# Kernel optimization log

Measured on AMD Instinct MI355X. Metric: run time of the kernel, lower is better.

## Reference

```python
import jax, jax.numpy as jnp
import numpy as np

B, N, NODE_DIM = 64, 64, 192
H = 256          # node_hidden_dim
PDIM = 64        # property_embedding_dim
NUM_EDGE_TYPE = 5
T = 4            # message-passing rounds
E = 16384        # total edges (flattened batched graph)
E_SEL = 65536    # selected candidate pairs


def setup_inputs() -> dict:
    key = jax.random.key(0)
    ks = jax.random.split(key, 24)
    def g(k, shape, scale=0.05):
        return jax.random.normal(k, shape, dtype=jnp.float32) * scale
    inp = {
        "x": jax.random.normal(ks[0], (B, N, NODE_DIM), dtype=jnp.float32),
        "edge_index": jax.random.randint(ks[1], (2, E), 0, B * N, dtype=jnp.int32),
        "edge_attr": jax.random.uniform(ks[2], (E, NUM_EDGE_TYPE), dtype=jnp.float32),
        "props": jax.random.normal(ks[3], (B, 1), dtype=jnp.float32),
        "sel_b": jax.random.randint(ks[4], (E_SEL,), 0, B, dtype=jnp.int32),
        "sel_i": jax.random.randint(ks[5], (E_SEL,), 0, N, dtype=jnp.int32),
        "sel_j": jax.random.randint(ks[6], (E_SEL,), 0, N, dtype=jnp.int32),
        "golden_edge": jax.random.randint(ks[7], (E_SEL,), 0, NUM_EDGE_TYPE, dtype=jnp.int32),
        # parameters
        "W_prop": g(ks[8], (1, PDIM)), "b_prop": jnp.zeros((PDIM,), jnp.float32),
        "W_in": g(ks[9], (NODE_DIM, H)), "b_in": jnp.zeros((H,), jnp.float32),
        "W_msg": g(ks[10], (H + NUM_EDGE_TYPE, H)), "b_msg": jnp.zeros((H,), jnp.float32),
        "W_upd": g(ks[11], (2 * H, H)), "b_upd": jnp.zeros((H,), jnp.float32),
        "W_add": g(ks[12], (H + PDIM, H)), "b_add": jnp.zeros((H,), jnp.float32),
        "W1": g(ks[13], (2 * H, H)), "b1": jnp.zeros((H,), jnp.float32),
        "W2": g(ks[14], (H, H)), "b2": jnp.zeros((H,), jnp.float32),
        "W3": g(ks[15], (H, 2 * H)), "b3": jnp.zeros((2 * H,), jnp.float32),
        "W_out": g(ks[16], (2 * H, NUM_EDGE_TYPE)), "b_out": jnp.zeros((NUM_EDGE_TYPE,), jnp.float32),
    }
    return inp


def reference(x, edge_index, edge_attr, props, sel_b, sel_i, sel_j, golden_edge,
              W_prop, b_prop, W_in, b_in, W_msg, b_msg, W_upd, b_upd,
              W_add, b_add, W1, b1, W2, b2, W3, b3, W_out, b_out):
    BN = B * N
    node_x = x.reshape(BN, NODE_DIM)
    src, dst = edge_index[0], edge_index[1]

    # --- GNN node embedding (t rounds of message passing, opaque Encoder.embed_node) ---
    h = jax.nn.relu(node_x @ W_in + b_in)                       # [BN, H]
    for _ in range(T):
        msg_in = jnp.concatenate([h[src], edge_attr], axis=-1)  # [E, H+num_edge_type]
        msg = jax.nn.relu(msg_in @ W_msg + b_msg)               # [E, H]
        agg = jax.ops.segment_sum(msg, dst, num_segments=BN)    # [BN, H]
        h = jax.nn.relu(jnp.concatenate([h, agg], axis=-1) @ W_upd + b_upd)

    node_emb = h.reshape(B, N, H)

    # --- property conditioning + addition linear ---
    prop = props @ W_prop + b_prop                               # [B, PDIM]
    propp = jnp.broadcast_to(prop[:, None, :], (B, N, PDIM))
    node_embg = jnp.concatenate([node_emb, propp], axis=-1) @ W_add + b_add  # [B, N, H]

    # --- gather selected (src, dst) pairs directly (equiv. to repeat_interleave + boolean mask) ---
    flat = node_embg.reshape(BN, H)
    src_e = flat[sel_b * N + sel_i]                              # [E_SEL, H]
    dst_e = flat[sel_b * N + sel_j]                              # [E_SEL, H]
    pair = jnp.concatenate([src_e, dst_e], axis=-1)              # [E_SEL, 2H]

    # --- edge predictor MLP (3 layers, ReLU between) + output linear ---
    h1 = jax.nn.relu(pair @ W1 + b1)
    h2 = jax.nn.relu(h1 @ W2 + b2)
    h3 = h2 @ W3 + b3
    logits = h3 @ W_out + b_out                                  # [E_SEL, num_edge_type]

    # --- cross entropy (mean) ---
    logp = jax.nn.log_softmax(logits, axis=-1)
    loss = -jnp.mean(jnp.take_along_axis(logp, golden_edge[:, None].astype(jnp.int32), axis=-1))
    return loss
```

## Files before the change

### kernel.cpp

```cpp
#include <hip/hip_runtime.h>
#include <math.h>

#define BN 4096
#define N_PER_B 64
#define NE 16384
#define NSEL 65536
#define NET 5
#define PD 64
#define H1STR 260
#define FSTR 264
#define PTILES 2

typedef float f32x4 __attribute__((ext_vector_type(4)));
typedef float f32x16 __attribute__((ext_vector_type(16)));
typedef short short8 __attribute__((ext_vector_type(8)));
typedef short short4v __attribute__((ext_vector_type(4)));

__device__ __forceinline__ unsigned short f2bf(float f) {
    unsigned int u = __builtin_bit_cast(unsigned int, f);
    u += 0x7fff + ((u >> 16) & 1);
    return (unsigned short)(u >> 16);
}
__device__ __forceinline__ float bf_lo(unsigned int u) {
    return __builtin_bit_cast(float, u << 16);
}
__device__ __forceinline__ float bf_hi(unsigned int u) {
    return __builtin_bit_cast(float, u & 0xffff0000u);
}
__device__ __forceinline__ unsigned int pack2(float a, float b) {
    return (unsigned)f2bf(a) | ((unsigned)f2bf(b) << 16);
}
__device__ __forceinline__ short8 ld_frag(const unsigned short* p) {
    const short4v lo = *(const short4v*)(p);
    const short4v hi = *(const short4v*)(p + 4);
    return __builtin_shufflevector(lo, hi, 0, 1, 2, 3, 4, 5, 6, 7);
}
__device__ __forceinline__ unsigned int addrelu2(unsigned int a, unsigned int b, unsigned int c) {
    const float lo = fmaxf(bf_lo(a) + bf_lo(b) + bf_lo(c), 0.f);
    const float hi = fmaxf(bf_hi(a) + bf_hi(b) + bf_hi(c), 0.f);
    return pack2(lo, hi);
}

__global__ __launch_bounds__(256) void k_hist(const int* __restrict__ eidx,
                                              int* __restrict__ deg)
{
    const int e = blockIdx.x * 256 + threadIdx.x;
    atomicAdd(&deg[eidx[NE + e]], 1);
}

__global__ __launch_bounds__(256) void csr_scan(const int* __restrict__ deg,
                                                int* __restrict__ row_start,
                                                int* __restrict__ cursor)
{
    __shared__ int sums[256];
    const int tid = threadIdx.x;
    const int base = tid * 16;
    int local[16];
    int s = 0;
    #pragma unroll
    for (int i = 0; i < 16; ++i) { local[i] = s; s += deg[base + i]; }
    sums[tid] = s;
    __syncthreads();
    for (int off = 1; off < 256; off <<= 1) {
        const int v = sums[tid];
        const int add = (tid >= off) ? sums[tid - off] : 0;
        __syncthreads();
        sums[tid] = v + add;
        __syncthreads();
    }
    const int offset = (tid == 0) ? 0 : sums[tid - 1];
    #pragma unroll
    for (int i = 0; i < 16; ++i) {
        const int v = offset + local[i];
        row_start[base + i] = v;
        cursor[base + i] = v;
    }
    if (tid == 255) row_start[4096] = NE;
}

__global__ __launch_bounds__(256) void csr_scatter(const int* __restrict__ eidx,
                                                   int* __restrict__ cursor,
                                                   int* __restrict__ srcs,
                                                   int* __restrict__ epos)
{
    const int e = blockIdx.x * 256 + threadIdx.x;
    const int pos = atomicAdd(&cursor[eidx[NE + e]], 1);
    srcs[pos] = eidx[e];
    epos[e] = pos;
}

__global__ __launch_bounds__(256) void k_pre(
    const float* __restrict__ W_in, const float* __restrict__ W_msg,
    const float* __restrict__ W_upd, const float* __restrict__ W_add,
    const float* __restrict__ W1, const float* __restrict__ W2,
    const float* __restrict__ W3, const float* __restrict__ b3,
    const float* __restrict__ W_out, const float* __restrict__ b_out,
    const float* __restrict__ props, const float* __restrict__ W_prop,
    const float* __restrict__ b_prop, const float* __restrict__ b_add,
    const float* __restrict__ b_msg, const float* __restrict__ eattr,
    const int* __restrict__ epos,
    unsigned short* __restrict__ wbf, unsigned short* __restrict__ WfT,
    float* __restrict__ bfv, float* __restrict__ prop_add,
    unsigned short* __restrict__ ETc)
{
    __shared__ __align__(16) char smem[16704];
    const int blk = blockIdx.x;
    const int tid = threadIdx.x;

    if (blk < 128) {
        float (*s)[65] = (float(*)[65])smem;
        const int wsel = blk >> 4;
        const int sub = blk & 15;
        const float* src; unsigned short* dst; int K = 256;
        switch (wsel) {
            case 0: src = W_in;              dst = wbf;                         K = 192; break;
            case 1: src = W_msg;             dst = wbf + 49152;                 break;
            case 2: src = W_upd;             dst = wbf + 49152 + 65536;         break;
            case 3: src = W_upd + 256 * 256; dst = wbf + 49152 + 2 * 65536;     break;
            case 4: src = W_add;             dst = wbf + 49152 + 3 * 65536;     break;
            case 5: src = W1;                dst = wbf + 49152 + 4 * 65536;     break;
            case 6: src = W1 + 256 * 256;    dst = wbf + 49152 + 5 * 65536;     break;
            default: src = W2;               dst = wbf + 49152 + 6 * 65536;     break;
        }
        const int k0 = (sub >> 2) * 64;
        const int n0 = (sub & 3) * 64;
        if (k0 >= K) return;
        const int tn = tid & 63;
        const int tg = tid >> 6;
        #pragma unroll
        for (int i = 0; i < 16; ++i) {
            const int kk = tg * 16 + i;
            s[kk][tn] = src[(size_t)(k0 + kk) * 256 + n0 + tn];
        }
        __syncthreads();
        #pragma unroll
        for (int i = 0; i < 16; ++i) {
            const int nn = tg * 16 + i;
            dst[(size_t)(n0 + nn) * K + k0 + tn] = f2bf(s[tn][nn]);
        }
    } else if (blk < 192) {
        const int b = blk - 128;
        const float pv = props[b];
        float acc = b_add[tid];
        for (int p = 0; p < PD; ++p) {
            const float e = fmaf(pv, W_prop[p], b_prop[p]);
            acc = fmaf(e, W_add[(256 + p) * 256 + tid], acc);
        }
        prop_add[b * 256 + tid] = acc;
    } else if (blk < 449) {
        float* part = (float*)smem;
        const int cb = blk - 192;
        float acc[NET] = {0.f, 0.f, 0.f, 0.f, 0.f};
        #pragma unroll
        for (int rep = 0; rep < 2; ++rep) {
            const int j = rep * 256 + tid;
            const float wv = (cb < 256) ? W3[(size_t)cb * 512 + j] : b3[j];
            #pragma unroll
            for (int t = 0; t < NET; ++t) acc[t] = fmaf(wv, W_out[j * NET + t], acc[t]);
        }
        #pragma unroll
        for (int t = 0; t < NET; ++t)
            for (int off = 32; off >= 1; off >>= 1) acc[t] += __shfl_down(acc[t], off);
        if ((tid & 63) == 0) {
            #pragma unroll
            for (int t = 0; t < NET; ++t) part[(tid >> 6) * NET + t] = acc[t];
        }
        __syncthreads();
        if (tid == 0) {
            float s[NET];
            #pragma unroll
            for (int t = 0; t < NET; ++t)
                s[t] = part[t] + part[NET + t] + part[2 * NET + t] + part[3 * NET + t];
            if (cb < 256) {
                #pragma unroll
                for (int t = 0; t < NET; ++t) WfT[t * 256 + cb] = f2bf(s[t]);
                #pragma unroll
                for (int t = NET; t < 16; ++t) WfT[t * 256 + cb] = 0;
            } else {
                #pragma unroll
                for (int t = 0; t < NET; ++t) bfv[t] = s[t] + b_out[t];
            }
        }
    } else {
        float* ea = (float*)smem;
        int* eposs = (int*)(smem + 2560 + 64);
        const int eb = (blk - 449) * 128;
        if (tid < 160)
            *(float4*)&ea[tid * 4] = *(const float4*)(eattr + (size_t)eb * 5 + tid * 4);
        if (tid < 128) eposs[tid] = epos[eb + tid];
        __syncthreads();
        const float* Wme = W_msg + 256 * 256;
        const float w0 = Wme[0 * 256 + tid];
        const float w1 = Wme[1 * 256 + tid];
        const float w2 = Wme[2 * 256 + tid];
        const float w3 = Wme[3 * 256 + tid];
        const float w4 = Wme[4 * 256 + tid];
        const float bm = b_msg[tid];
        for (int i = 0; i < 128; ++i) {
            const float* a = ea + i * 5;
            float v = bm;
            v = fmaf(a[0], w0, v); v = fmaf(a[1], w1, v); v = fmaf(a[2], w2, v);
            v = fmaf(a[3], w3, v); v = fmaf(a[4], w4, v);
            ETc[(size_t)eposs[i] * 256 + tid] = f2bf(v);
        }
    }
}

__global__ __launch_bounds__(1024) void fstep(
    const float* __restrict__ x, const unsigned short* __restrict__ hbuf,
    const unsigned short* __restrict__ Pin, const unsigned short* __restrict__ ETc,
    const int* __restrict__ row_start, const int* __restrict__ srcs,
    const unsigned short* __restrict__ WaT, const unsigned short* __restrict__ WbT,
    const float* __restrict__ bias1,
    const unsigned short* __restrict__ Wp2T, const float* __restrict__ prop_add,
    const unsigned short* __restrict__ W1aT, const unsigned short* __restrict__ W1bT,
    unsigned short* __restrict__ hout, unsigned short* __restrict__ out1,
    unsigned short* __restrict__ out2, int mode)
{
    __shared__ __align__(16) unsigned short Hg[16 * FSTR];
    __shared__ __align__(16) unsigned short Ag[16 * FSTR];
    __shared__ __align__(16) unsigned short Hs[16 * FSTR];
    __shared__ __align__(16) unsigned short H2s[16 * FSTR];
    const int tid = threadIdx.x;
    const int w = tid >> 6;
    const int lane = tid & 63;
    const int q = lane >> 4;
    const int tx = lane & 15;
    const int m0 = blockIdx.x * 16;
    const int col = w * 16 + tx;

    if (mode != 0) {
        {
            const int r = tid >> 6;
            const int c4 = (tid & 63) * 4;
            *(uint2*)&Hg[r * FSTR + c4] =
                *(const uint2*)(hbuf + (size_t)(m0 + r) * 256 + c4);
        }
        {
            const int node = m0 + w;
            const int beg = row_start[node];
            const int end = row_start[node + 1];
            const int c = lane * 4;
            float a0 = 0.f, a1 = 0.f, a2 = 0.f, a3 = 0.f;
            for (int idx = beg; idx < end; ++idx) {
                const int src = srcs[idx];
                const uint2 pu = *(const uint2*)(Pin + (size_t)src * 256 + c);
                const uint2 eu = *(const uint2*)(ETc + (size_t)idx * 256 + c);
                a0 += fmaxf(bf_lo(pu.x) + bf_lo(eu.x), 0.f);
                a1 += fmaxf(bf_hi(pu.x) + bf_hi(eu.x), 0.f);
                a2 += fmaxf(bf_lo(pu.y) + bf_lo(eu.y), 0.f);
                a3 += fmaxf(bf_hi(pu.y) + bf_hi(eu.y), 0.f);
            }
            uint2 o; o.x = pack2(a0, a1); o.y = pack2(a2, a3);
            *(uint2*)&Ag[w * FSTR + c] = o;
        }
        __syncthreads();
    }

    f32x4 acc = (f32x4)0.f;
    if (mode == 0) {
        #pragma unroll
        for (int s = 0; s < 6; ++s) {
            const int k0 = s * 32;
            const float* ap = x + (size_t)(m0 + tx) * 192 + k0 + q * 8;
            const float4 v0 = *(const float4*)ap;
            const float4 v1 = *(const float4*)(ap + 4);
            short8 af;
            af[0] = (short)f2bf(v0.x); af[1] = (short)f2bf(v0.y);
            af[2] = (short)f2bf(v0.z); af[3] = (short)f2bf(v0.w);
            af[4] = (short)f2bf(v1.x); af[5] = (short)f2bf(v1.y);
            af[6] = (short)f2bf(v1.z); af[7] = (short)f2bf(v1.w);
            const short8 bfr = *(const short8*)(WaT + (size_t)col * 192 + k0 + q * 8);
            acc = __builtin_amdgcn_mfma_f32_16x16x32_bf16(af, bfr, acc, 0, 0, 0);
        }
    } else {
        #pragma unroll
        for (int s = 0; s < 8; ++s) {
            const int k0 = s * 32;
            const short8 af = *(const short8*)&Hg[tx * FSTR + k0 + q * 8];
            const short8 bfr = *(const short8*)(WaT + (size_t)col * 256 + k0 + q * 8);
            acc = __builtin_amdgcn_mfma_f32_16x16x32_bf16(af, bfr, acc, 0, 0, 0);
        }
        #pragma unroll
        for (int s = 0; s < 8; ++s) {
            const int k0 = s * 32;
            const short8 af = *(const short8*)&Ag[tx * FSTR + k0 + q * 8];
            const short8 bfr = *(const short8*)(WbT + (size_t)col * 256 + k0 + q * 8);
            acc = __builtin_amdgcn_mfma_f32_16x16x32_bf16(af, bfr, acc, 0, 0, 0);
        }
    }
    {
        const float bv = bias1[col];
        #pragma unroll
        for (int r = 0; r < 4; ++r) {
            const int row = q * 4 + r;
            const unsigned short us = f2bf(fmaxf(acc[r] + bv, 0.f));
            Hs[row * FSTR + col] = us;
            if (mode < 2) hout[(size_t)(m0 + row) * 256 + col] = us;
        }
    }
    __syncthreads();

    acc = (f32x4)0.f;
    #pragma unroll
    for (int s = 0; s < 8; ++s) {
        const int k0 = s * 32;
        const short8 af = *(const short8*)&Hs[tx * FSTR + k0 + q * 8];
        const short8 bfr = *(const short8*)(Wp2T + (size_t)col * 256 + k0 + q * 8);
        acc = __builtin_amdgcn_mfma_f32_16x16x32_bf16(af, bfr, acc, 0, 0, 0);
    }
    if (mode < 2) {
        #pragma unroll
        for (int r = 0; r < 4; ++r)
            out1[(size_t)(m0 + q * 4 + r) * 256 + col] = f2bf(acc[r]);
        return;
    }
    {
        const float pv = prop_add[(m0 >> 6) * 256 + col];
        #pragma unroll
        for (int r = 0; r < 4; ++r)
            H2s[(q * 4 + r) * FSTR + col] = f2bf(acc[r] + pv);
    }
    __syncthreads();

    for (int which = 0; which < 2; ++which) {
        const unsigned short* WT = which ? W1bT : W1aT;
        unsigned short* op = which ? out2 : out1;
        acc = (f32x4)0.f;
        #pragma unroll
        for (int s = 0; s < 8; ++s) {
            const int k0 = s * 32;
            const short8 af = *(const short8*)&H2s[tx * FSTR + k0 + q * 8];
            const short8 bfr = *(const short8*)(WT + (size_t)col * 256 + k0 + q * 8);
            acc = __builtin_amdgcn_mfma_f32_16x16x32_bf16(af, bfr, acc, 0, 0, 0);
        }
        #pragma unroll
        for (int r = 0; r < 4; ++r)
            op[(size_t)(m0 + q * 4 + r) * 256 + col] = f2bf(acc[r]);
    }
}

__global__ __launch_bounds__(512, 2) void pair_k(
    const unsigned short* __restrict__ A1t, const unsigned short* __restrict__ A2t,
    const float* __restrict__ b1, const unsigned short* __restrict__ W2T,
    const float* __restrict__ b2, const unsigned short* __restrict__ WfT,
    const float* __restrict__ bfv,
    const int* __restrict__ sel_b, const int* __restrict__ sel_i,
    const int* __restrict__ sel_j, const int* __restrict__ golden,
    float* __restrict__ out)
{
    __shared__ __align__(16) unsigned short sbuf[64 * H1STR];
    __shared__ __align__(16) unsigned short b1s[256];
    __shared__ float Lg[64 * 8];
    __shared__ int sidx[64 * PTILES], didx[64 * PTILES], gold[64 * PTILES];

    const int tid = threadIdx.x;
    const int w = tid >> 6;
    const int lane = tid & 63;
    const int q = lane >> 4;
    const int tx = lane & 15;
    const int m = lane & 31;
    const int hh = lane >> 5;
    const int e0 = blockIdx.x * 64 * PTILES;

    if (tid < 64 * PTILES) {
        const int e = e0 + tid;
        const int b = sel_b[e];
        sidx[tid] = b * N_PER_B + sel_i[e];
        didx[tid] = b * N_PER_B + sel_j[e];
        gold[tid] = golden[e];
    }
    if (tid < 256) b1s[tid] = f2bf(b1[tid]);

    short8 Breg[16];
    {
        const unsigned short* bb = W2T + (size_t)(w * 32 + m) * 256 + hh * 8;
        #pragma unroll
        for (int s = 0; s < 16; ++s)
            Breg[s] = *(const short8*)(bb + s * 16);
    }
    __syncthreads();

    float total = 0.f;

    for (int t = 0; t < PTILES; ++t) {
        {
            const int hw = tid >> 5;
            #pragma unroll
            for (int j = 0; j < 4; ++j) {
                const int p = j * 16 + hw;
                const unsigned short* r1 = A1t + (size_t)sidx[t * 64 + p] * 256 + m * 8;
                const unsigned short* r2 = A2t + (size_t)didx[t * 64 + p] * 256 + m * 8;
                const uint4 u1 = *(const uint4*)r1;
                const uint4 u2 = *(const uint4*)r2;
                const uint4 ub = *(const uint4*)(b1s + m * 8);
                uint2 lo2, hi2;
                lo2.x = addrelu2(u1.x, u2.x, ub.x);
                lo2.y = addrelu2(u1.y, u2.y, ub.y);
                hi2.x = addrelu2(u1.z, u2.z, ub.z);
                hi2.y = addrelu2(u1.w, u2.w, ub.w);
                unsigned short* dbase = sbuf + p * H1STR + m * 8;
                *(uint2*)(dbase) = lo2;
                *(uint2*)(dbase + 4) = hi2;
            }
        }
        __syncthreads();

        f32x16 acc0 = (f32x16)0.f;
        f32x16 acc1 = (f32x16)0.f;
        {
            const unsigned short* a0row = sbuf + (size_t)m * H1STR + hh * 8;
            const unsigned short* a1row = a0row + 32 * H1STR;
            #pragma unroll
            for (int s = 0; s < 16; ++s) {
                const short8 af0 = ld_frag(a0row + s * 16);
                acc0 = __builtin_amdgcn_mfma_f32_32x32x16_bf16(af0, Breg[s], acc0, 0, 0, 0);
                const short8 af1 = ld_frag(a1row + s * 16);
                acc1 = __builtin_amdgcn_mfma_f32_32x32x16_bf16(af1, Breg[s], acc1, 0, 0, 0);
            }
        }
        __syncthreads();

        {
            const int col = w * 32 + m;
            const float bv = b2[col];
            #pragma unroll
            for (int reg = 0; reg < 16; ++reg) {
                const int prow = (reg & 3) + 8 * (reg >> 2) + 4 * hh;
                sbuf[prow * H1STR + col] = f2bf(fmaxf(acc0[reg] + bv, 0.f));
                sbuf[(32 + prow) * H1STR + col] = f2bf(fmaxf(acc1[reg] + bv, 0.f));
            }
        }
        __syncthreads();

        if (w < 4) {
            f32x4 accL = (f32x4)0.f;
            const unsigned short* a2row = sbuf + (size_t)(w * 16 + tx) * H1STR + q * 8;
            const unsigned short* bWf = WfT + (size_t)tx * 256 + q * 8;
            #pragma unroll
            for (int s = 0; s < 8; ++s) {
                const short8 af = ld_frag(a2row + s * 32);
                const short8 bfr = *(const short8*)(bWf + s * 32);
                accL = __builtin_amdgcn_mfma_f32_16x16x32_bf16(af, bfr, accL, 0, 0, 0);
            }
            if (tx < NET) {
                const float bb = bfv[tx];
                #pragma unroll
                for (int reg = 0; reg < 4; ++reg)
                    Lg[(w * 16 + q * 4 + reg) * 8 + tx] = accL[reg] + bb;
            }
        }
        __syncthreads();

        if (tid < 64) {
            float lg[NET];
            #pragma unroll
            for (int tt = 0; tt < NET; ++tt) lg[tt] = Lg[tid * 8 + tt];
            float mx = lg[0];
            #pragma unroll
            for (int tt = 1; tt < NET; ++tt) mx = fmaxf(mx, lg[tt]);
            float s = 0.f;
            #pragma unroll
            for (int tt = 0; tt < NET; ++tt) s += expf(lg[tt] - mx);
            float ls = mx + logf(s) - lg[gold[t * 64 + tid]];
            #pragma unroll
            for (int off = 32; off >= 1; off >>= 1) ls += __shfl_xor(ls, off);
            total += ls;
        }
        __syncthreads();
    }

    if (tid == 0) atomicAdd(out, total * (1.0f / NSEL));
}

extern "C" void kernel_launch(void* const* d_in, const int* in_sizes, int n_in,
                              void* d_out, int out_size, void* d_ws, size_t ws_size,
                              hipStream_t stream) {
    (void)in_sizes; (void)n_in; (void)out_size; (void)ws_size;
    const float* x      = (const float*)d_in[0];
    const int*   eidx   = (const int*)d_in[1];
    const float* eattr  = (const float*)d_in[2];
    const float* props  = (const float*)d_in[3];
    const int*   sel_b  = (const int*)d_in[4];
    const int*   sel_i  = (const int*)d_in[5];
    const int*   sel_j  = (const int*)d_in[6];
    const int*   golden = (const int*)d_in[7];
    const float* W_prop = (const float*)d_in[8];
    const float* b_prop = (const float*)d_in[9];
    const float* W_in   = (const float*)d_in[10];
    const float* b_in   = (const float*)d_in[11];
    const float* W_msg  = (const float*)d_in[12];
    const float* b_msg  = (const float*)d_in[13];
    const float* W_upd  = (const float*)d_in[14];
    const float* b_upd  = (const float*)d_in[15];
    const float* W_add  = (const float*)d_in[16];
    const float* b_add  = (const float*)d_in[17];
    const float* W1     = (const float*)d_in[18];
    const float* b1     = (const float*)d_in[19];
    const float* W2     = (const float*)d_in[20];
    const float* b2     = (const float*)d_in[21];
    const float* W3     = (const float*)d_in[22];
    const float* b3     = (const float*)d_in[23];
    const float* W_out  = (const float*)d_in[24];
    const float* b_out  = (const float*)d_in[25];

    const size_t SEG = (size_t)BN * 256;
    unsigned short* P0   = (unsigned short*)d_ws;
    unsigned short* P1   = P0 + SEG;
    unsigned short* hA   = P1 + SEG;
    unsigned short* hB   = hA + SEG;
    unsigned short* ETc  = hB + SEG;
    unsigned short* wbf  = ETc + (size_t)NE * 256;
    unsigned short* W_inT  = wbf;
    unsigned short* WmT    = wbf + 49152;
    unsigned short* WuaT   = WmT + 65536;
    unsigned short* WubT   = WuaT + 65536;
    unsigned short* W_addT = WubT + 65536;
    unsigned short* W1aT   = W_addT + 65536;
    unsigned short* W1bT   = W1aT + 65536;
    unsigned short* W2T    = W1bT + 65536;
    unsigned short* WfT    = W2T + 65536;
    float* prop_add = (float*)(WfT + 4096);
    float* bfv = prop_add + 64 * 256;
    int* deg       = (int*)(bfv + 16);
    int* row_start = deg + 4096;
    int* cursor    = row_start + 4104;
    int* srcs      = cursor + 4096;
    int* epos      = srcs + NE;

    hipMemsetAsync(deg, 0, 4096 * sizeof(int), stream);
    k_hist<<<NE / 256, 256, 0, stream>>>(eidx, deg);
    csr_scan<<<1, 256, 0, stream>>>(deg, row_start, cursor);
    csr_scatter<<<NE / 256, 256, 0, stream>>>(eidx, cursor, srcs, epos);
    k_pre<<<577, 256, 0, stream>>>(W_in, W_msg, W_upd, W_add, W1, W2, W3, b3,
                                   W_out, b_out, props, W_prop, b_prop, b_add,
                                   b_msg, eattr, epos, wbf, WfT, bfv, prop_add, ETc);

    fstep<<<256, 1024, 0, stream>>>(x, nullptr, nullptr, ETc, row_start, srcs,
                                    W_inT, nullptr, b_in, WmT, nullptr, nullptr, nullptr,
                                    hA, P0, nullptr, 0);
    fstep<<<256, 1024, 0, stream>>>(nullptr, hA, P0, ETc, row_start, srcs,
                                    WuaT, WubT, b_upd, WmT, nullptr, nullptr, nullptr,
                                    hB, P1, nullptr, 1);
    fstep<<<256, 1024, 0, stream>>>(nullptr, hB, P1, ETc, row_start, srcs,
                                    WuaT, WubT, b_upd, WmT, nullptr, nullptr, nullptr,
                                    hA, P0, nullptr, 1);
    fstep<<<256, 1024, 0, stream>>>(nullptr, hA, P0, ETc, row_start, srcs,
                                    WuaT, WubT, b_upd, WmT, nullptr, nullptr, nullptr,
                                    hB, P1, nullptr, 1);
    fstep<<<256, 1024, 0, stream>>>(nullptr, hB, P1, ETc, row_start, srcs,
                                    WuaT, WubT, b_upd, W_addT, prop_add, W1aT, W1bT,
                                    nullptr, P0, hA, 2);

    hipMemsetAsync(d_out, 0, sizeof(float), stream);
    pair_k<<<NSEL / (64 * PTILES), 512, 0, stream>>>(P0, hA, b1, W2T, b2, WfT, bfv,
                                    sel_b, sel_i, sel_j, golden, (float*)d_out);
}
```

Baseline: 254.2 us.

## Fuse CSR build into one kernel, fold output memset, unroll edge gather

Replaces the memset, histogram, single-block scan and scatter kernels with one 64-block kernel. Each block scans all destinations, counts edges that fall below its 64-node range to get its starting offset, and scatters its own edges using shared-memory atomics. The output zeroing moves into k_pre so one memset launch disappears, and the message-aggregation gather loop is unrolled by four so more loads are in flight. The trade-off is that every CSR block reads the whole edge list twice, the scatter order inside a node stays nondeterministic, and float summation order changes.

```diff
diff --git a/kernel.cpp b/kernel.cpp
--- a/kernel.cpp
+++ b/kernel.cpp
@@ -41,52 +41,55 @@
     return pack2(lo, hi);
 }
 
-__global__ __launch_bounds__(256) void k_hist(const int* __restrict__ eidx,
-                                              int* __restrict__ deg)
+__global__ __launch_bounds__(256) void csr_fused(const int* __restrict__ eidx,
+                                                 int* __restrict__ row_start,
+                                                 int* __restrict__ srcs,
+                                                 int* __restrict__ epos)
 {
-    const int e = blockIdx.x * 256 + threadIdx.x;
-    atomicAdd(&deg[eidx[NE + e]], 1);
-}
-
-__global__ __launch_bounds__(256) void csr_scan(const int* __restrict__ deg,
-                                                int* __restrict__ row_start,
-                                                int* __restrict__ cursor)
-{
-    __shared__ int sums[256];
+    __shared__ int own[64];
+    __shared__ int red[256];
     const int tid = threadIdx.x;
-    const int base = tid * 16;
-    int local[16];
-    int s = 0;
-    #pragma unroll
-    for (int i = 0; i < 16; ++i) { local[i] = s; s += deg[base + i]; }
-    sums[tid] = s;
+    const int blk = blockIdx.x;
+    const int lo = blk * 64;
+
+    if (tid < 64) own[tid] = 0;
     __syncthreads();
-    for (int off = 1; off < 256; off <<= 1) {
-        const int v = sums[tid];
-        const int add = (tid >= off) ? sums[tid - off] : 0;
-        __syncthreads();
-        sums[tid] = v + add;
-        __syncthreads();
-    }
-    const int offset = (tid == 0) ? 0 : sums[tid - 1];
-    #pragma unroll
-    for (int i = 0; i < 16; ++i) {
-        const int v = offset + local[i];
-        row_start[base + i] = v;
-        cursor[base + i] = v;
-    }
-    if (tid == 255) row_start[4096] = NE;
-}
-
-__global__ __launch_bounds__(256) void csr_scatter(const int* __restrict__ eidx,
-                                                   int* __restrict__ cursor,
-                                                   int* __restrict__ srcs,
-                                                   int* __restrict__ epos)
-{
-    const int e = blockIdx.x * 256 + threadIdx.x;
-    const int pos = atomicAdd(&cursor[eidx[NE + e]], 1);
-    srcs[pos] = eidx[e];
-    epos[e] = pos;
+
+    int cnt = 0;
+    #pragma unroll 4
+    for (int i = 0; i < 64; ++i) {
+        const int d = eidx[NE + i * 256 + tid];
+        if (d < lo) ++cnt;
+        else if (d < lo + 64) atomicAdd(&own[d - lo], 1);
+    }
+    red[tid] = cnt;
+    __syncthreads();
+    for (int off = 128; off >= 1; off >>= 1) {
+        if (tid < off) red[tid] += red[tid + off];
+        __syncthreads();
+    }
+    if (tid == 0) {
+        int acc = red[0];
+        for (int i = 0; i < 64; ++i) {
+            const int d = own[i];
+            own[i] = acc;
+            row_start[lo + i] = acc;
+            acc += d;
+        }
+        if (blk == 63) row_start[4096] = NE;
+    }
+    __syncthreads();
+
+    #pragma unroll 4
+    for (int i = 0; i < 64; ++i) {
+        const int e = i * 256 + tid;
+        const int d = eidx[NE + e];
+        if (d >= lo && d < lo + 64) {
+            const int pos = atomicAdd(&own[d - lo], 1);
+            srcs[pos] = eidx[e];
+            epos[e] = pos;
+        }
+    }
 }
 
 __global__ __launch_bounds__(256) void k_pre(
@@ -101,11 +104,13 @@
     const int* __restrict__ epos,
     unsigned short* __restrict__ wbf, unsigned short* __restrict__ WfT,
     float* __restrict__ bfv, float* __restrict__ prop_add,
-    unsigned short* __restrict__ ETc)
+    unsigned short* __restrict__ ETc, float* __restrict__ out)
 {
     __shared__ __align__(16) char smem[16704];
     const int blk = blockIdx.x;
     const int tid = threadIdx.x;
+
+    if (blk == 0 && tid == 0) out[0] = 0.f;
 
     if (blk < 128) {
         float (*s)[65] = (float(*)[65])smem;
@@ -242,7 +247,28 @@
             const int end = row_start[node + 1];
             const int c = lane * 4;
             float a0 = 0.f, a1 = 0.f, a2 = 0.f, a3 = 0.f;
-            for (int idx = beg; idx < end; ++idx) {
+            int idx = beg;
+            for (; idx + 3 < end; idx += 4) {
+                const int s0 = srcs[idx], s1 = srcs[idx + 1];
+                const int s2 = srcs[idx + 2], s3 = srcs[idx + 3];
+                const uint2 p0 = *(const uint2*)(Pin + (size_t)s0 * 256 + c);
+                const uint2 p1 = *(const uint2*)(Pin + (size_t)s1 * 256 + c);
+                const uint2 p2 = *(const uint2*)(Pin + (size_t)s2 * 256 + c);
+                const uint2 p3 = *(const uint2*)(Pin + (size_t)s3 * 256 + c);
+                const uint2 e0 = *(const uint2*)(ETc + (size_t)idx * 256 + c);
+                const uint2 e1 = *(const uint2*)(ETc + (size_t)(idx + 1) * 256 + c);
+                const uint2 e2 = *(const uint2*)(ETc + (size_t)(idx + 2) * 256 + c);
+                const uint2 e3 = *(const uint2*)(ETc + (size_t)(idx + 3) * 256 + c);
+                a0 += fmaxf(bf_lo(p0.x) + bf_lo(e0.x), 0.f) + fmaxf(bf_lo(p1.x) + bf_lo(e1.x), 0.f)
+                    + fmaxf(bf_lo(p2.x) + bf_lo(e2.x), 0.f) + fmaxf(bf_lo(p3.x) + bf_lo(e3.x), 0.f);
+                a1 += fmaxf(bf_hi(p0.x) + bf_hi(e0.x), 0.f) + fmaxf(bf_hi(p1.x) + bf_hi(e1.x), 0.f)
+                    + fmaxf(bf_hi(p2.x) + bf_hi(e2.x), 0.f) + fmaxf(bf_hi(p3.x) + bf_hi(e3.x), 0.f);
+                a2 += fmaxf(bf_lo(p0.y) + bf_lo(e0.y), 0.f) + fmaxf(bf_lo(p1.y) + bf_lo(e1.y), 0.f)
+                    + fmaxf(bf_lo(p2.y) + bf_lo(e2.y), 0.f) + fmaxf(bf_lo(p3.y) + bf_lo(e3.y), 0.f);
+                a3 += fmaxf(bf_hi(p0.y) + bf_hi(e0.y), 0.f) + fmaxf(bf_hi(p1.y) + bf_hi(e1.y), 0.f)
+                    + fmaxf(bf_hi(p2.y) + bf_hi(e2.y), 0.f) + fmaxf(bf_hi(p3.y) + bf_hi(e3.y), 0.f);
+            }
+            for (; idx < end; ++idx) {
                 const int src = srcs[idx];
                 const uint2 pu = *(const uint2*)(Pin + (size_t)src * 256 + c);
                 const uint2 eu = *(const uint2*)(ETc + (size_t)idx * 256 + c);
@@ -522,19 +548,15 @@
     unsigned short* WfT    = W2T + 65536;
     float* prop_add = (float*)(WfT + 4096);
     float* bfv = prop_add + 64 * 256;
-    int* deg       = (int*)(bfv + 16);
-    int* row_start = deg + 4096;
-    int* cursor    = row_start + 4104;
-    int* srcs      = cursor + 4096;
+    int* row_start = (int*)(bfv + 16);
+    int* srcs      = row_start + 4104;
     int* epos      = srcs + NE;
 
-    hipMemsetAsync(deg, 0, 4096 * sizeof(int), stream);
-    k_hist<<<NE / 256, 256, 0, stream>>>(eidx, deg);
-    csr_scan<<<1, 256, 0, stream>>>(deg, row_start, cursor);
-    csr_scatter<<<NE / 256, 256, 0, stream>>>(eidx, cursor, srcs, epos);
+    csr_fused<<<64, 256, 0, stream>>>(eidx, row_start, srcs, epos);
     k_pre<<<577, 256, 0, stream>>>(W_in, W_msg, W_upd, W_add, W1, W2, W3, b3,
                                    W_out, b_out, props, W_prop, b_prop, b_add,
-                                   b_msg, eattr, epos, wbf, WfT, bfv, prop_add, ETc);
+                                   b_msg, eattr, epos, wbf, WfT, bfv, prop_add,
+                                   ETc, (float*)d_out);
 
     fstep<<<256, 1024, 0, stream>>>(x, nullptr, nullptr, ETc, row_start, srcs,
                                     W_inT, nullptr, b_in, WmT, nullptr, nullptr, nullptr,
@@ -552,7 +574,6 @@
                                     WuaT, WubT, b_upd, W_addT, prop_add, W1aT, W1bT,
                                     nullptr, P0, hA, 2);
 
-    hipMemsetAsync(d_out, 0, sizeof(float), stream);
     pair_k<<<NSEL / (64 * PTILES), 512, 0, stream>>>(P0, hA, b1, W2T, b2, WfT, bfv,
                                     sel_b, sel_i, sel_j, golden, (float*)d_out);
 }
```

Result: slower. 273.3 us (+7.5%).

## Pack edge id into CSR source, fold memsets into k_pre, unroll aggregation

Applied to the files above, without the earlier changes.

The CSR scatter now packs the source node and the original edge id into one int, so ETc is written in original edge order and k_pre no longer depends on the scatter output. The two memsets (degree histogram and output scalar) are folded into k_pre, which now runs first, removing two launches and the epos array. The neighbor aggregation loop in fstep is unrolled by four to issue more independent gathers, at the cost of non-sequential ETc reads indexed by edge id.

```diff
diff --git a/kernel.cpp b/kernel.cpp
--- a/kernel.cpp
+++ b/kernel.cpp
@@ -80,13 +80,11 @@
 
 __global__ __launch_bounds__(256) void csr_scatter(const int* __restrict__ eidx,
                                                    int* __restrict__ cursor,
-                                                   int* __restrict__ srcs,
-                                                   int* __restrict__ epos)
+                                                   int* __restrict__ srcs)
 {
     const int e = blockIdx.x * 256 + threadIdx.x;
     const int pos = atomicAdd(&cursor[eidx[NE + e]], 1);
-    srcs[pos] = eidx[e];
-    epos[e] = pos;
+    srcs[pos] = eidx[e] | (e << 12);
 }
 
 __global__ __launch_bounds__(256) void k_pre(
@@ -98,14 +96,17 @@
     const float* __restrict__ props, const float* __restrict__ W_prop,
     const float* __restrict__ b_prop, const float* __restrict__ b_add,
     const float* __restrict__ b_msg, const float* __restrict__ eattr,
-    const int* __restrict__ epos,
     unsigned short* __restrict__ wbf, unsigned short* __restrict__ WfT,
     float* __restrict__ bfv, float* __restrict__ prop_add,
-    unsigned short* __restrict__ ETc)
+    unsigned short* __restrict__ ETc, float* __restrict__ out,
+    int* __restrict__ deg)
 {
     __shared__ __align__(16) char smem[16704];
     const int blk = blockIdx.x;
     const int tid = threadIdx.x;
+
+    if (blk < 16) deg[blk * 256 + tid] = 0;
+    if (blk == 0 && tid == 0) out[0] = 0.f;
 
     if (blk < 128) {
         float (*s)[65] = (float(*)[65])smem;
@@ -183,11 +184,9 @@
         }
     } else {
         float* ea = (float*)smem;
-        int* eposs = (int*)(smem + 2560 + 64);
         const int eb = (blk - 449) * 128;
         if (tid < 160)
             *(float4*)&ea[tid * 4] = *(const float4*)(eattr + (size_t)eb * 5 + tid * 4);
-        if (tid < 128) eposs[tid] = epos[eb + tid];
         __syncthreads();
         const float* Wme = W_msg + 256 * 256;
         const float w0 = Wme[0 * 256 + tid];
@@ -201,7 +200,7 @@
             float v = bm;
             v = fmaf(a[0], w0, v); v = fmaf(a[1], w1, v); v = fmaf(a[2], w2, v);
             v = fmaf(a[3], w3, v); v = fmaf(a[4], w4, v);
-            ETc[(size_t)eposs[i] * 256 + tid] = f2bf(v);
+            ETc[(size_t)(eb + i) * 256 + tid] = f2bf(v);
         }
     }
 }
@@ -242,10 +241,31 @@
             const int end = row_start[node + 1];
             const int c = lane * 4;
             float a0 = 0.f, a1 = 0.f, a2 = 0.f, a3 = 0.f;
-            for (int idx = beg; idx < end; ++idx) {
-                const int src = srcs[idx];
-                const uint2 pu = *(const uint2*)(Pin + (size_t)src * 256 + c);
-                const uint2 eu = *(const uint2*)(ETc + (size_t)idx * 256 + c);
+            int idx = beg;
+            for (; idx + 3 < end; idx += 4) {
+                const int k0 = srcs[idx],     k1 = srcs[idx + 1];
+                const int k2 = srcs[idx + 2], k3 = srcs[idx + 3];
+                const uint2 p0 = *(const uint2*)(Pin + (size_t)(k0 & 4095) * 256 + c);
+                const uint2 p1 = *(const uint2*)(Pin + (size_t)(k1 & 4095) * 256 + c);
+                const uint2 p2 = *(const uint2*)(Pin + (size_t)(k2 & 4095) * 256 + c);
+                const uint2 p3 = *(const uint2*)(Pin + (size_t)(k3 & 4095) * 256 + c);
+                const uint2 e0 = *(const uint2*)(ETc + (size_t)(k0 >> 12) * 256 + c);
+                const uint2 e1 = *(const uint2*)(ETc + (size_t)(k1 >> 12) * 256 + c);
+                const uint2 e2 = *(const uint2*)(ETc + (size_t)(k2 >> 12) * 256 + c);
+                const uint2 e3 = *(const uint2*)(ETc + (size_t)(k3 >> 12) * 256 + c);
+                a0 += fmaxf(bf_lo(p0.x) + bf_lo(e0.x), 0.f) + fmaxf(bf_lo(p1.x) + bf_lo(e1.x), 0.f)
+                    + fmaxf(bf_lo(p2.x) + bf_lo(e2.x), 0.f) + fmaxf(bf_lo(p3.x) + bf_lo(e3.x), 0.f);
+                a1 += fmaxf(bf_hi(p0.x) + bf_hi(e0.x), 0.f) + fmaxf(bf_hi(p1.x) + bf_hi(e1.x), 0.f)
+                    + fmaxf(bf_hi(p2.x) + bf_hi(e2.x), 0.f) + fmaxf(bf_hi(p3.x) + bf_hi(e3.x), 0.f);
+                a2 += fmaxf(bf_lo(p0.y) + bf_lo(e0.y), 0.f) + fmaxf(bf_lo(p1.y) + bf_lo(e1.y), 0.f)
+                    + fmaxf(bf_lo(p2.y) + bf_lo(e2.y), 0.f) + fmaxf(bf_lo(p3.y) + bf_lo(e3.y), 0.f);
+                a3 += fmaxf(bf_hi(p0.y) + bf_hi(e0.y), 0.f) + fmaxf(bf_hi(p1.y) + bf_hi(e1.y), 0.f)
+                    + fmaxf(bf_hi(p2.y) + bf_hi(e2.y), 0.f) + fmaxf(bf_hi(p3.y) + bf_hi(e3.y), 0.f);
+            }
+            for (; idx < end; ++idx) {
+                const int pk = srcs[idx];
+                const uint2 pu = *(const uint2*)(Pin + (size_t)(pk & 4095) * 256 + c);
+                const uint2 eu = *(const uint2*)(ETc + (size_t)(pk >> 12) * 256 + c);
                 a0 += fmaxf(bf_lo(pu.x) + bf_lo(eu.x), 0.f);
                 a1 += fmaxf(bf_hi(pu.x) + bf_hi(eu.x), 0.f);
                 a2 += fmaxf(bf_lo(pu.y) + bf_lo(eu.y), 0.f);
@@ -522,19 +542,18 @@
     unsigned short* WfT    = W2T + 65536;
     float* prop_add = (float*)(WfT + 4096);
     float* bfv = prop_add + 64 * 256;
-    int* deg       = (int*)(bfv + 16);
-    int* row_start = deg + 4096;
-    int* cursor    = row_start + 4104;
-    int* srcs      = cursor + 4096;
-    int* epos      = srcs + NE;
-
-    hipMemsetAsync(deg, 0, 4096 * sizeof(int), stream);
+    int* row_start = (int*)(bfv + 16);
+    int* srcs      = row_start + 4104;
+    int* deg       = srcs + NE;
+    int* cursor    = deg + 4096;
+
+    k_pre<<<577, 256, 0, stream>>>(W_in, W_msg, W_upd, W_add, W1, W2, W3, b3,
+                                   W_out, b_out, props, W_prop, b_prop, b_add,
+                                   b_msg, eattr, wbf, WfT, bfv, prop_add,
+                                   ETc, (float*)d_out, deg);
     k_hist<<<NE / 256, 256, 0, stream>>>(eidx, deg);
     csr_scan<<<1, 256, 0, stream>>>(deg, row_start, cursor);
-    csr_scatter<<<NE / 256, 256, 0, stream>>>(eidx, cursor, srcs, epos);
-    k_pre<<<577, 256, 0, stream>>>(W_in, W_msg, W_upd, W_add, W1, W2, W3, b3,
-                                   W_out, b_out, props, W_prop, b_prop, b_add,
-                                   b_msg, eattr, epos, wbf, WfT, bfv, prop_add, ETc);
+    csr_scatter<<<NE / 256, 256, 0, stream>>>(eidx, cursor, srcs);
 
     fstep<<<256, 1024, 0, stream>>>(x, nullptr, nullptr, ETc, row_start, srcs,
                                     W_inT, nullptr, b_in, WmT, nullptr, nullptr, nullptr,
@@ -552,7 +571,6 @@
                                     WuaT, WubT, b_upd, W_addT, prop_add, W1aT, W1bT,
                                     nullptr, P0, hA, 2);
 
-    hipMemsetAsync(d_out, 0, sizeof(float), stream);
     pair_k<<<NSEL / (64 * PTILES), 512, 0, stream>>>(P0, hA, b1, W2T, b2, WfT, bfv,
                                     sel_b, sel_i, sel_j, golden, (float*)d_out);
 }
```

New measurement: 245.0 us. 1.04x faster.
